# Kernel tuning notes

Hardware: AMD Instinct MI355X
Metric: run time of the kernel (lower is better)

## Reference

```python
import jax, jax.numpy as jnp
import numpy as np

N = 10000       # nodes
E = 200000      # node pairs (edges) in rel_dict
R = 400000      # relation instances
F_IN = 128
F_OUT = 64


def setup_inputs() -> dict:
    key = jax.random.key(0)
    ks = jax.random.split(key, 8)
    x = jax.random.normal(ks[0], (N, F_IN), dtype=jnp.float32)
    rel = jax.random.normal(ks[1], (R, F_IN), dtype=jnp.float32)
    adj = jax.random.uniform(ks[2], (N, N), dtype=jnp.float32)
    edge_pairs = jax.random.randint(ks[3], (E, 2), 0, N, dtype=jnp.int32)
    rel_seg = jax.random.randint(ks[4], (R,), 0, E, dtype=jnp.int32)
    # Conv1d(in, out, kernel_size=1, bias=False) == Linear: weight [out, in]
    W = jax.random.normal(ks[5], (F_OUT, F_IN), dtype=jnp.float32) * 0.1
    w_rel = jax.random.normal(ks[6], (F_IN,), dtype=jnp.float32) * 0.1
    bias = jnp.zeros((F_OUT,), dtype=jnp.float32)
    return {"x": x, "rel": rel, "adj": adj, "edge_pairs": edge_pairs,
            "rel_seg": rel_seg, "W": W, "w_rel": w_rel, "bias": bias}


def reference(x, rel, adj, edge_pairs, rel_seg, W, w_rel, bias):
    # node transform: [N, F_OUT]
    seq_fts = x @ W.T
    # per-relation scalar: [R]
    fts_rel = rel @ w_rel
    # segment-mean per edge (vectorized form of the rel_dict loop)
    sums = jax.ops.segment_sum(fts_rel, rel_seg, num_segments=E)
    cnts = jax.ops.segment_sum(jnp.ones_like(fts_rel), rel_seg, num_segments=E)
    edge_means = sums / jnp.maximum(cnts, 1.0)  # [E]
    # symmetric scatter into dense logits [N, N]
    e1, e2 = edge_pairs[:, 0], edge_pairs[:, 1]
    logits = jnp.zeros_like(adj)
    logits = logits.at[e1, e2].set(edge_means).at[e2, e1].set(edge_means)
    # masked-ish softmax over rows, then sparse-weighted aggregation
    coefs = jax.nn.softmax(jax.nn.sigmoid(logits) + adj, axis=1)  # [N, N]
    # dropout is a no-op in eval mode (training=False)
    ret = coefs @ seq_fts + bias  # [N, F_OUT]
    return jax.nn.elu(ret)        # concat=True
```

## Files before the change

kernel.cpp:

```cpp
#include <hip/hip_runtime.h>
#include <math.h>

#define NN   10000
#define EE   200000
#define RR   400000
#define FIN  128
#define FOUT 64

#define HASH_BITS 20
#define HSIZE (1u << HASH_BITS)
#define HMASK (HSIZE - 1u)
#define ROWCAP 256

#define NKB 314
#define NC  20
#define CHKF 512
#define LDSP 520

typedef __bf16 bf16x8 __attribute__((ext_vector_type(8)));
typedef __bf16 bf16x4 __attribute__((ext_vector_type(4)));
typedef float  f32x4  __attribute__((ext_vector_type(4)));

#define O_SUMS   0
#define O_CNTS   (O_SUMS + EE)
#define O_ROWCNT (O_CNTS + EE)
#define O_HKEY   (O_ROWCNT + NN)
#define O_HPRIO  (O_HKEY + HSIZE)
#define O_SEQTP  (O_HPRIO + HSIZE)
#define SEQTP_WORDS (NKB * 5 * 512 / 2)
#define ZERO_WORDS (O_SEQTP + SEQTP_WORDS)
#define O_NUMP   ZERO_WORDS
#define O_SP     (O_NUMP + 4 * NN * FOUT)
#define O_PAIRS  (O_SP + 4 * NN)

__global__ __launch_bounds__(256) void k_zero(f32x4* __restrict__ p, int n4) {
    int gid = blockIdx.x * 256 + threadIdx.x;
    if (gid < n4) p[gid] = (f32x4){0.f, 0.f, 0.f, 0.f};
}

__global__ __launch_bounds__(256) void k_seqfts(const float* __restrict__ x,
                                                const float* __restrict__ W,
                                                __bf16* __restrict__ seqTp) {
    __shared__ float Wt[FIN][FOUT + 1];
    __shared__ float xs[FIN][16 + 1];
    int t = threadIdx.x;
    for (int e = t; e < FOUT * FIN; e += 256) {
        int c = e >> 7, k = e & 127;
        Wt[k][c] = W[e];
    }
    int row0 = blockIdx.x * 16;
    for (int e = t; e < 16 * FIN; e += 256) {
        int r = e >> 7, k = e & 127;
        int gr = row0 + r;
        xs[k][r] = (gr < NN) ? x[(size_t)gr * FIN + k] : 0.f;
    }
    __syncthreads();
    int col = t & 63;
    int rg  = t >> 6;
    float acc[4] = {0.f, 0.f, 0.f, 0.f};
    for (int k = 0; k < FIN; ++k) {
        float w = Wt[k][col];
        #pragma unroll
        for (int i = 0; i < 4; ++i) acc[i] += w * xs[k][rg * 4 + i];
    }
    #pragma unroll
    for (int i = 0; i < 4; ++i) {
        int gr = row0 + rg * 4 + i;
        int kb = gr >> 5, g = (gr >> 3) & 3, slot = gr & 7;
        seqTp[((size_t)kb * 5 + (col >> 4)) * 512 + ((col & 15) + g * 16) * 8 + slot]
            = (__bf16)acc[i];
        if (col < 16)
            seqTp[((size_t)kb * 5 + 4) * 512 + (col + g * 16) * 8 + slot] = (__bf16)1.0f;
    }
}

__device__ __forceinline__ unsigned hash_cell(unsigned cell) {
    return (cell * 2654435761u) >> (32 - HASH_BITS);
}
__device__ __forceinline__ void entry_ij(const int* ep, int e, int& i, int& j, int& k) {
    k = (e < EE) ? e : e - EE;
    int a = ep[2 * k], b = ep[2 * k + 1];
    if (e < EE) { i = a; j = b; } else { i = b; j = a; }
}

__global__ __launch_bounds__(256) void k_hash(const int* __restrict__ ep,
                                              unsigned* __restrict__ hkey,
                                              unsigned* __restrict__ hprio) {
    int e = blockIdx.x * 256 + threadIdx.x;
    if (e >= 2 * EE) return;
    int i, j, k;
    entry_ij(ep, e, i, j, k);
    unsigned cell = (unsigned)i * NN + (unsigned)j;
    unsigned keyv = cell + 1u;
    unsigned h = hash_cell(cell);
    while (true) {
        unsigned old = atomicCAS(&hkey[h], 0u, keyv);
        if (old == 0u || old == keyv) break;
        h = (h + 1u) & HMASK;
    }
    atomicMax(&hprio[h], (unsigned)(e + 1));
}

#define RELBLK 2048
__global__ __launch_bounds__(256) void k_rel(const float* __restrict__ rel,
                                             const float* __restrict__ wrel,
                                             const int* __restrict__ rseg,
                                             float* __restrict__ sums,
                                             float* __restrict__ cnts) {
    int t = threadIdx.x;
    int wv = blockIdx.x * 4 + (t >> 6);
    int l = t & 63;
    int lane = l & 31, half = l >> 5;
    f32x4 wvv = *(const f32x4*)(wrel + lane * 4);
    const int NW2 = RELBLK * 4 * 2;
    for (int base = wv * 2; base < RR; base += NW2) {
        int row = base + half;
        f32x4 v = *(const f32x4*)(rel + (size_t)row * FIN + lane * 4);
        float s = v.x * wvv.x + v.y * wvv.y + v.z * wvv.z + v.w * wvv.w;
        s += __shfl_xor(s, 1, 64);
        s += __shfl_xor(s, 2, 64);
        s += __shfl_xor(s, 4, 64);
        s += __shfl_xor(s, 8, 64);
        s += __shfl_xor(s, 16, 64);
        if (lane == 0) {
            int seg = rseg[row];
            atomicAdd(&sums[seg], s);
            atomicAdd(&cnts[seg], 1.0f);
        }
    }
}

__global__ __launch_bounds__(256) void k_main(const float* __restrict__ adj,
                                              const __bf16* __restrict__ seqTp,
                                              float* __restrict__ Nump,
                                              float* __restrict__ Sp) {
    __shared__ __bf16 As[2][16][LDSP];
    int t = threadIdx.x;
    int w = t >> 6, l = t & 63;
    int row0 = blockIdx.x * 16;
    int lr = l & 15, lk = l >> 4;

    f32x4 acc[5];
    #pragma unroll
    for (int n = 0; n < 5; ++n) acc[n] = (f32x4){0.f, 0.f, 0.f, 0.f};

    f32x4 pv[8];
    #pragma unroll
    for (int r = 0; r < 4; ++r) {
        const float* ap = adj + (size_t)(row0 + w * 4 + r) * NN;
        pv[2 * r]     = *(const f32x4*)(ap + 4 * l);
        pv[2 * r + 1] = *(const f32x4*)(ap + 256 + 4 * l);
    }

    int p = 0;
    for (int c = 0; c < NC; ++c) {
        #pragma unroll
        for (int r = 0; r < 4; ++r) {
            #pragma unroll
            for (int h2 = 0; h2 < 2; ++h2) {
                f32x4 v = pv[2 * r + h2];
                float e0 = exp2f(fmaf(v.x, 1.442695041f, 0.7213475204f));
                float e1 = exp2f(fmaf(v.y, 1.442695041f, 0.7213475204f));
                float e2 = exp2f(fmaf(v.z, 1.442695041f, 0.7213475204f));
                float e3 = exp2f(fmaf(v.w, 1.442695041f, 0.7213475204f));
                bf16x4 q = { (__bf16)e0, (__bf16)e1, (__bf16)e2, (__bf16)e3 };
                *(bf16x4*)&As[p][w * 4 + r][h2 * 256 + 4 * l] = q;
            }
        }
        if (c + 1 < NC) {
            int kn = (c + 1) * CHKF;
            #pragma unroll
            for (int r = 0; r < 4; ++r) {
                const float* ap = adj + (size_t)(row0 + w * 4 + r) * NN + kn;
                pv[2 * r] = *(const f32x4*)(ap + 4 * l);
                int g1 = kn + 256 + 4 * l;
                pv[2 * r + 1] = (g1 < NN) ? *(const f32x4*)(ap + 256 + 4 * l)
                                          : (f32x4){-1e9f, -1e9f, -1e9f, -1e9f};
            }
        }
        __syncthreads();
        int kb0 = (c * CHKF) >> 5;
        #pragma unroll
        for (int h = 0; h < 4; ++h) {
            int kb = kb0 + w * 4 + h;
            if (kb < NKB) {
                bf16x8 af = *(const bf16x8*)&As[p][lr][w * 128 + h * 32 + lk * 8];
                const __bf16* bp = seqTp + (size_t)kb * 5 * 512 + l * 8;
                #pragma unroll
                for (int n = 0; n < 5; ++n) {
                    bf16x8 b = *(const bf16x8*)(bp + n * 512);
                    acc[n] = __builtin_amdgcn_mfma_f32_16x16x32_bf16(af, b, acc[n], 0, 0, 0);
                }
            }
        }
        p ^= 1;
    }

    float* nout = Nump + (size_t)w * NN * FOUT;
    #pragma unroll
    for (int n = 0; n < 4; ++n) {
        #pragma unroll
        for (int r = 0; r < 4; ++r)
            nout[(size_t)(row0 + lk * 4 + r) * FOUT + n * 16 + lr] = acc[n][r];
    }
    if (lr == 0) {
        #pragma unroll
        for (int r = 0; r < 4; ++r)
            Sp[(size_t)w * NN + row0 + lk * 4 + r] = acc[4][r];
    }
}

__global__ __launch_bounds__(256) void k_scatB(const int* __restrict__ ep,
                                               const float* __restrict__ sums,
                                               const float* __restrict__ cnts,
                                               const unsigned* __restrict__ hkey,
                                               const unsigned* __restrict__ hprio,
                                               const float* __restrict__ adj,
                                               int* __restrict__ rowcnt,
                                               uint2* __restrict__ pairs) {
    int e = blockIdx.x * 256 + threadIdx.x;
    if (e >= 2 * EE) return;
    int i, j, k;
    entry_ij(ep, e, i, j, k);
    unsigned cell = (unsigned)i * NN + (unsigned)j;
    unsigned keyv = cell + 1u;
    unsigned h = hash_cell(cell);
    while (hkey[h] != keyv) h = (h + 1u) & HMASK;
    if (hprio[h] == (unsigned)(e + 1)) {
        float v   = sums[k] / fmaxf(cnts[k], 1.0f);
        float sg  = 1.f / (1.f + __expf(-v));
        float aij = adj[(size_t)i * NN + j];
        float dw  = __expf(aij + sg) - __expf(aij + 0.5f);
        if (dw != 0.f) {
            int pos = atomicAdd(&rowcnt[i], 1);
            if (pos < ROWCAP)
                pairs[(size_t)i * ROWCAP + pos] =
                    make_uint2((unsigned)j, __float_as_uint(dw));
        }
    }
}

__global__ __launch_bounds__(256) void k_rowupd(const float* __restrict__ Nump,
                                                const float* __restrict__ Sp,
                                                const int* __restrict__ rowcnt,
                                                const uint2* __restrict__ pairs,
                                                const __bf16* __restrict__ seqTp,
                                                const float* __restrict__ bias,
                                                float* __restrict__ out) {
    int t = threadIdx.x;
    int i = blockIdx.x * 4 + (t >> 6);
    if (i >= NN) return;
    int c = t & 63;
    float acc = 0.f, sb = 0.f;
    #pragma unroll
    for (int ks = 0; ks < 4; ++ks) {
        acc += Nump[(size_t)ks * NN * FOUT + (size_t)i * FOUT + c];
        sb  += Sp[(size_t)ks * NN + i];
    }
    int cnt = min(rowcnt[i], ROWCAP);
    float sdw = 0.f;
    const uint2* pr = pairs + (size_t)i * ROWCAP;
    for (int e = 0; e < cnt; ++e) {
        uint2 pk = pr[e];
        float d  = __uint_as_float(pk.y);
        unsigned j = pk.x;
        float sj = (float)seqTp[((size_t)(j >> 5) * 5 + (c >> 4)) * 512
                                + ((c & 15) + ((j >> 3) & 3) * 16) * 8 + (j & 7)];
        acc += d * sj;
        sdw += d;
    }
    float v = acc / (sb + sdw) + bias[c];
    out[(size_t)i * FOUT + c] = (v > 0.f) ? v : expm1f(v);
}

extern "C" void kernel_launch(void* const* d_in, const int* in_sizes, int n_in,
                              void* d_out, int out_size, void* d_ws, size_t ws_size,
                              hipStream_t stream) {
    const float* x    = (const float*)d_in[0];
    const float* rel  = (const float*)d_in[1];
    const float* adj  = (const float*)d_in[2];
    const int*   ep   = (const int*)d_in[3];
    const int*   rseg = (const int*)d_in[4];
    const float* W    = (const float*)d_in[5];
    const float* wrel = (const float*)d_in[6];
    const float* bias = (const float*)d_in[7];
    float* out = (float*)d_out;

    float* ws = (float*)d_ws;
    float*    sums   = ws + O_SUMS;
    float*    cnts   = ws + O_CNTS;
    int*      rowcnt = (int*)(ws + O_ROWCNT);
    unsigned* hkey   = (unsigned*)(ws + O_HKEY);
    unsigned* hprio  = (unsigned*)(ws + O_HPRIO);
    __bf16*   seqTp  = (__bf16*)(ws + O_SEQTP);
    float*    Nump   = ws + O_NUMP;
    float*    Sp     = ws + O_SP;
    uint2*    pairs  = (uint2*)(ws + O_PAIRS);

    int n4 = ZERO_WORDS / 4;
    k_zero<<<(n4 + 255) / 256, 256, 0, stream>>>((f32x4*)d_ws, n4);
    k_seqfts<<<NN / 16, 256, 0, stream>>>(x, W, seqTp);
    k_hash<<<(2 * EE + 255) / 256, 256, 0, stream>>>(ep, hkey, hprio);
    k_rel<<<RELBLK, 256, 0, stream>>>(rel, wrel, rseg, sums, cnts);
    k_main<<<NN / 16, 256, 0, stream>>>(adj, seqTp, Nump, Sp);
    k_scatB<<<(2 * EE + 255) / 256, 256, 0, stream>>>(ep, sums, cnts, hkey, hprio,
                                                      adj, rowcnt, pairs);
    k_rowupd<<<(NN + 3) / 4, 256, 0, stream>>>(Nump, Sp, rowcnt, pairs,
                                               seqTp, bias, out);
}
```

Before: 315.6 us.

## Fuse hash, relation reduction and main GEMM into one interleaved kernel

Merges the hash-build, relation segment-sum and dense adj-softmax GEMM kernels into a single launch, interleaving relation-reduction blocks between main blocks and appending hash blocks. The main part now uses 512-thread blocks with 8 waves, each handling two k-blocks per chunk, so the partial sums grow to 8 slices that the row-update kernel reduces. The intent is to overlap the memory-bound relation and atomic hash work with the adj-streaming GEMM and cut launch gaps. In exchange it doubles the partial-output traffic, and the larger blocks may affect occupancy.

```diff
diff --git a/kernel.cpp b/kernel.cpp
--- a/kernel.cpp
+++ b/kernel.cpp
@@ -13,9 +13,6 @@
 #define ROWCAP 256
 
 #define NKB 314
-#define NC  20
-#define CHKF 512
-#define LDSP 520
 
 typedef __bf16 bf16x8 __attribute__((ext_vector_type(8)));
 typedef __bf16 bf16x4 __attribute__((ext_vector_type(4)));
@@ -30,8 +27,8 @@
 #define SEQTP_WORDS (NKB * 5 * 512 / 2)
 #define ZERO_WORDS (O_SEQTP + SEQTP_WORDS)
 #define O_NUMP   ZERO_WORDS
-#define O_SP     (O_NUMP + 4 * NN * FOUT)
-#define O_PAIRS  (O_SP + 4 * NN)
+#define O_SP     (O_NUMP + 8 * NN * FOUT)
+#define O_PAIRS  (O_SP + 8 * NN)
 
 __global__ __launch_bounds__(256) void k_zero(f32x4* __restrict__ p, int n4) {
     int gid = blockIdx.x * 256 + threadIdx.x;
@@ -83,108 +80,114 @@
     if (e < EE) { i = a; j = b; } else { i = b; j = a; }
 }
 
-__global__ __launch_bounds__(256) void k_hash(const int* __restrict__ ep,
-                                              unsigned* __restrict__ hkey,
-                                              unsigned* __restrict__ hprio) {
-    int e = blockIdx.x * 256 + threadIdx.x;
-    if (e >= 2 * EE) return;
-    int i, j, k;
-    entry_ij(ep, e, i, j, k);
-    unsigned cell = (unsigned)i * NN + (unsigned)j;
-    unsigned keyv = cell + 1u;
-    unsigned h = hash_cell(cell);
-    while (true) {
-        unsigned old = atomicCAS(&hkey[h], 0u, keyv);
-        if (old == 0u || old == keyv) break;
-        h = (h + 1u) & HMASK;
-    }
-    atomicMax(&hprio[h], (unsigned)(e + 1));
-}
-
-#define RELBLK 2048
-__global__ __launch_bounds__(256) void k_rel(const float* __restrict__ rel,
-                                             const float* __restrict__ wrel,
-                                             const int* __restrict__ rseg,
-                                             float* __restrict__ sums,
-                                             float* __restrict__ cnts) {
-    int t = threadIdx.x;
-    int wv = blockIdx.x * 4 + (t >> 6);
-    int l = t & 63;
-    int lane = l & 31, half = l >> 5;
-    f32x4 wvv = *(const f32x4*)(wrel + lane * 4);
-    const int NW2 = RELBLK * 4 * 2;
-    for (int base = wv * 2; base < RR; base += NW2) {
-        int row = base + half;
-        f32x4 v = *(const f32x4*)(rel + (size_t)row * FIN + lane * 4);
-        float s = v.x * wvv.x + v.y * wvv.y + v.z * wvv.z + v.w * wvv.w;
-        s += __shfl_xor(s, 1, 64);
-        s += __shfl_xor(s, 2, 64);
-        s += __shfl_xor(s, 4, 64);
-        s += __shfl_xor(s, 8, 64);
-        s += __shfl_xor(s, 16, 64);
-        if (lane == 0) {
-            int seg = rseg[row];
-            atomicAdd(&sums[seg], s);
-            atomicAdd(&cnts[seg], 1.0f);
-        }
-    }
-}
-
-__global__ __launch_bounds__(256) void k_main(const float* __restrict__ adj,
-                                              const __bf16* __restrict__ seqTp,
-                                              float* __restrict__ Nump,
-                                              float* __restrict__ Sp) {
+#define NC 20
+#define CHKF 512
+#define LDSP 520
+#define MAINBLK 625
+#define ILV 11
+#define MRB (ILV * MAINBLK)
+#define HASHB ((2 * EE + 511) / 512)
+#define GRID_MR (MRB + HASHB)
+
+__global__ __launch_bounds__(512) void k_mr(const float* __restrict__ adj,
+                                            const __bf16* __restrict__ seqTp,
+                                            const float* __restrict__ rel,
+                                            const float* __restrict__ wrel,
+                                            const int* __restrict__ rseg,
+                                            const int* __restrict__ ep,
+                                            float* __restrict__ sums,
+                                            float* __restrict__ cnts,
+                                            unsigned* __restrict__ hkey,
+                                            unsigned* __restrict__ hprio,
+                                            float* __restrict__ Nump,
+                                            float* __restrict__ Sp) {
     __shared__ __bf16 As[2][16][LDSP];
-    int t = threadIdx.x;
-    int w = t >> 6, l = t & 63;
-    int row0 = blockIdx.x * 16;
+    int t   = threadIdx.x;
+    int bid = blockIdx.x;
+
+    if (bid >= MRB) {
+        int e = (bid - MRB) * 512 + t;
+        if (e >= 2 * EE) return;
+        int i, j, k;
+        entry_ij(ep, e, i, j, k);
+        unsigned cell = (unsigned)i * NN + (unsigned)j;
+        unsigned keyv = cell + 1u;
+        unsigned h = hash_cell(cell);
+        while (true) {
+            unsigned old = atomicCAS(&hkey[h], 0u, keyv);
+            if (old == 0u || old == keyv) break;
+            h = (h + 1u) & HMASK;
+        }
+        atomicMax(&hprio[h], (unsigned)(e + 1));
+        return;
+    }
+
+    if (bid % ILV) {
+        int relb = bid - bid / ILV - 1;
+        int lane = t & 31;
+        f32x4 wv = *(const f32x4*)(wrel + lane * 4);
+        int rbase = relb * 64 + (t >> 5);
+        #pragma unroll
+        for (int pass = 0; pass < 4; ++pass) {
+            int row = rbase + pass * 16;
+            f32x4 v = *(const f32x4*)(rel + (size_t)row * FIN + lane * 4);
+            float s = v.x * wv.x + v.y * wv.y + v.z * wv.z + v.w * wv.w;
+            #pragma unroll
+            for (int off = 16; off >= 1; off >>= 1) s += __shfl_xor(s, off, 64);
+            if (lane == 0) {
+                int seg = rseg[row];
+                atomicAdd(&sums[seg], s);
+                atomicAdd(&cnts[seg], 1.0f);
+            }
+        }
+        return;
+    }
+
+    int mi   = bid / ILV;
+    int row0 = mi * 16;
+    int w  = t >> 6, l = t & 63;
     int lr = l & 15, lk = l >> 4;
+    int sr = t >> 5;
+    int sq = t & 31;
+    const float* arow = adj + (size_t)(row0 + sr) * NN;
 
     f32x4 acc[5];
     #pragma unroll
     for (int n = 0; n < 5; ++n) acc[n] = (f32x4){0.f, 0.f, 0.f, 0.f};
 
-    f32x4 pv[8];
-    #pragma unroll
-    for (int r = 0; r < 4; ++r) {
-        const float* ap = adj + (size_t)(row0 + w * 4 + r) * NN;
-        pv[2 * r]     = *(const f32x4*)(ap + 4 * l);
-        pv[2 * r + 1] = *(const f32x4*)(ap + 256 + 4 * l);
-    }
-
+    f32x4 pv[4];
+#define LOADW(CH)                                                          \
+    {                                                                      \
+        int kbase = (CH) * CHKF + sq * 4;                                  \
+        _Pragma("unroll")                                                  \
+        for (int s = 0; s < 4; ++s) {                                      \
+            int gk = kbase + s * 128;                                      \
+            pv[s] = (gk < NN) ? *(const f32x4*)(arow + gk)                 \
+                              : (f32x4){-1e9f, -1e9f, -1e9f, -1e9f};      \
+        }                                                                  \
+    }
+
+    LOADW(0);
     int p = 0;
     for (int c = 0; c < NC; ++c) {
         #pragma unroll
-        for (int r = 0; r < 4; ++r) {
-            #pragma unroll
-            for (int h2 = 0; h2 < 2; ++h2) {
-                f32x4 v = pv[2 * r + h2];
-                float e0 = exp2f(fmaf(v.x, 1.442695041f, 0.7213475204f));
-                float e1 = exp2f(fmaf(v.y, 1.442695041f, 0.7213475204f));
-                float e2 = exp2f(fmaf(v.z, 1.442695041f, 0.7213475204f));
-                float e3 = exp2f(fmaf(v.w, 1.442695041f, 0.7213475204f));
-                bf16x4 q = { (__bf16)e0, (__bf16)e1, (__bf16)e2, (__bf16)e3 };
-                *(bf16x4*)&As[p][w * 4 + r][h2 * 256 + 4 * l] = q;
-            }
-        }
-        if (c + 1 < NC) {
-            int kn = (c + 1) * CHKF;
-            #pragma unroll
-            for (int r = 0; r < 4; ++r) {
-                const float* ap = adj + (size_t)(row0 + w * 4 + r) * NN + kn;
-                pv[2 * r] = *(const f32x4*)(ap + 4 * l);
-                int g1 = kn + 256 + 4 * l;
-                pv[2 * r + 1] = (g1 < NN) ? *(const f32x4*)(ap + 256 + 4 * l)
-                                          : (f32x4){-1e9f, -1e9f, -1e9f, -1e9f};
-            }
-        }
+        for (int s = 0; s < 4; ++s) {
+            f32x4 v = pv[s];
+            float e0 = exp2f(fmaf(v.x, 1.442695041f, 0.7213475204f));
+            float e1 = exp2f(fmaf(v.y, 1.442695041f, 0.7213475204f));
+            float e2 = exp2f(fmaf(v.z, 1.442695041f, 0.7213475204f));
+            float e3 = exp2f(fmaf(v.w, 1.442695041f, 0.7213475204f));
+            bf16x4 q = { (__bf16)e0, (__bf16)e1, (__bf16)e2, (__bf16)e3 };
+            *(bf16x4*)&As[p][sr][sq * 4 + s * 128] = q;
+        }
+        if (c + 1 < NC) LOADW(c + 1);
         __syncthreads();
-        int kb0 = (c * CHKF) >> 5;
-        #pragma unroll
-        for (int h = 0; h < 4; ++h) {
-            int kb = kb0 + w * 4 + h;
+        int kb0 = c * 16;
+        #pragma unroll
+        for (int h = 0; h < 2; ++h) {
+            int kb = kb0 + w * 2 + h;
             if (kb < NKB) {
-                bf16x8 af = *(const bf16x8*)&As[p][lr][w * 128 + h * 32 + lk * 8];
+                bf16x8 af = *(const bf16x8*)&As[p][lr][(w * 2 + h) * 32 + lk * 8];
                 const __bf16* bp = seqTp + (size_t)kb * 5 * 512 + l * 8;
                 #pragma unroll
                 for (int n = 0; n < 5; ++n) {
@@ -195,6 +198,7 @@
         }
         p ^= 1;
     }
+#undef LOADW
 
     float* nout = Nump + (size_t)w * NN * FOUT;
     #pragma unroll
@@ -253,7 +257,7 @@
     int c = t & 63;
     float acc = 0.f, sb = 0.f;
     #pragma unroll
-    for (int ks = 0; ks < 4; ++ks) {
+    for (int ks = 0; ks < 8; ++ks) {
         acc += Nump[(size_t)ks * NN * FOUT + (size_t)i * FOUT + c];
         sb  += Sp[(size_t)ks * NN + i];
     }
@@ -300,9 +304,8 @@
     int n4 = ZERO_WORDS / 4;
     k_zero<<<(n4 + 255) / 256, 256, 0, stream>>>((f32x4*)d_ws, n4);
     k_seqfts<<<NN / 16, 256, 0, stream>>>(x, W, seqTp);
-    k_hash<<<(2 * EE + 255) / 256, 256, 0, stream>>>(ep, hkey, hprio);
-    k_rel<<<RELBLK, 256, 0, stream>>>(rel, wrel, rseg, sums, cnts);
-    k_main<<<NN / 16, 256, 0, stream>>>(adj, seqTp, Nump, Sp);
+    k_mr<<<GRID_MR, 512, 0, stream>>>(adj, seqTp, rel, wrel, rseg, ep,
+                                      sums, cnts, hkey, hprio, Nump, Sp);
     k_scatB<<<(2 * EE + 255) / 256, 256, 0, stream>>>(ep, sums, cnts, hkey, hprio,
                                                       adj, rowcnt, pairs);
     k_rowupd<<<(NN + 3) / 4, 256, 0, stream>>>(Nump, Sp, rowcnt, pairs,
```

Result: no change. 318.8 us (+1.0%).
